# Optimization experiments

Hardware: AMD Instinct MI355X
Metric: run time of the kernel (lower is better)

The kernel has to match this reference:

```python
import jax, jax.numpy as jnp
import numpy as np

D_MODEL = 1024
N_HEADS = 16
HEAD_DIM = D_MODEL // N_HEADS
EPS = 1e-5


def _rope_tables(T, dim, dtype):
    inv_freq = 1.0 / (10000.0 ** (np.arange(0, dim, 2, dtype=np.float32) / dim))
    t = np.arange(T, dtype=np.float32)
    freqs = np.einsum('i,j->ij', t, inv_freq)            # [T, dim/2]
    emb = np.concatenate([freqs, freqs], axis=-1)        # [T, dim]
    return jnp.asarray(np.cos(emb), dtype), jnp.asarray(np.sin(emb), dtype)


def _rotate(x, cos, sin):
    # x: [B, T, H, hd]; cos/sin: [T, hd] broadcast over B, H
    c = cos[None, :, None, :]
    s = sin[None, :, None, :]
    x1, x2 = jnp.split(x, 2, axis=-1)
    return x * c + jnp.concatenate([-x2, x1], axis=-1) * s


def setup_inputs() -> dict:
    key = jax.random.key(0)
    k1, k2, k3 = jax.random.split(key, 3)
    B, T = 2, 2048
    x = jax.random.normal(k1, (B, T, D_MODEL), jnp.float32)
    norm_w = jnp.ones((D_MODEL,), jnp.float32)
    w_qkv = jax.random.normal(k2, (D_MODEL, 3 * D_MODEL), jnp.float32) * (D_MODEL ** -0.5)
    w_out = jax.random.normal(k3, (D_MODEL, D_MODEL), jnp.float32) * (D_MODEL ** -0.5)
    return {"x": x, "norm_w": norm_w, "w_qkv": w_qkv, "w_out": w_out}


def reference(x, norm_w, w_qkv, w_out):
    B, T, D = x.shape
    residual = x
    # RMSNorm
    h = x * jax.lax.rsqrt(jnp.mean(x * x, axis=-1, keepdims=True) + EPS) * norm_w
    # QKV projection
    qkv = (h @ w_qkv).reshape(B, T, 3, N_HEADS, HEAD_DIM)
    q, k, v = qkv[:, :, 0], qkv[:, :, 1], qkv[:, :, 2]   # [B, T, H, hd]
    # RoPE
    cos, sin = _rope_tables(T, HEAD_DIM, x.dtype)
    q = _rotate(q, cos, sin)
    k = _rotate(k, cos, sin)
    # Non-causal scaled dot-product attention
    scale = HEAD_DIM ** -0.5
    scores = jnp.einsum('bqhd,bkhd->bhqk', q, k) * scale
    attn = jax.nn.softmax(scores, axis=-1)
    out = jnp.einsum('bhqk,bkhd->bqhd', attn, v).reshape(B, T, D)
    return residual + out @ w_out
```

## Files before the change

kernel.cpp:

```cpp
#include <hip/hip_runtime.h>
#include <hip/hip_bf16.h>

typedef float f32x4 __attribute__((ext_vector_type(4)));
typedef __bf16 bf16x8 __attribute__((ext_vector_type(8)));
typedef __bf16 bf16x4 __attribute__((ext_vector_type(4)));

#define D_MODEL 1024
#define T_SEQ   2048
#define NH      16
#define HD      64

__device__ __forceinline__ void gload16(const void* g, void* l) {
    __builtin_amdgcn_global_load_lds(
        (const __attribute__((address_space(1))) unsigned int*)g,
        (__attribute__((address_space(3))) unsigned int*)l, 16, 0, 0);
}

__global__ __launch_bounds__(256) void k_rope_table(float2* __restrict__ tab) {
    int idx = blockIdx.x * 256 + threadIdx.x;
    int t = idx >> 5, i = idx & 31;
    float inv = __builtin_amdgcn_exp2f(-(float)i * 0.41524101186f);
    float ang = (float)t * inv;
    tab[idx] = make_float2(cosf(ang), sinf(ang));
}

__global__ __launch_bounds__(256) void k_rmsnorm(const float* __restrict__ x,
                                                 const float* __restrict__ w,
                                                 __bf16* __restrict__ h) {
    int row = blockIdx.x;
    int tid = threadIdx.x;
    const float4 v = ((const float4*)(x + (size_t)row * D_MODEL))[tid];
    float ss = v.x * v.x + v.y * v.y + v.z * v.z + v.w * v.w;
#pragma unroll
    for (int off = 32; off > 0; off >>= 1) ss += __shfl_down(ss, off, 64);
    __shared__ float red[4];
    if ((tid & 63) == 0) red[tid >> 6] = ss;
    __syncthreads();
    float total = red[0] + red[1] + red[2] + red[3];
    float rms = rsqrtf(total * (1.f / 1024.f) + 1e-5f);
    const float4 wv = ((const float4*)w)[tid];
    bf16x4 o;
    o[0] = (__bf16)(v.x * rms * wv.x);
    o[1] = (__bf16)(v.y * rms * wv.y);
    o[2] = (__bf16)(v.z * rms * wv.z);
    o[3] = (__bf16)(v.w * rms * wv.w);
    ((bf16x4*)(h + (size_t)row * D_MODEL))[tid] = o;
}

__global__ __launch_bounds__(256) void k_transpose_cast(const float* __restrict__ src,
                                                        __bf16* __restrict__ dst,
                                                        int R, int C) {
    __shared__ float tile[32][33];
    int tx = threadIdx.x & 31, ty = threadIdx.x >> 5;
    int c0 = blockIdx.x * 32, r0 = blockIdx.y * 32;
#pragma unroll
    for (int dy = 0; dy < 32; dy += 8)
        tile[ty + dy][tx] = src[(size_t)(r0 + ty + dy) * C + c0 + tx];
    __syncthreads();
#pragma unroll
    for (int dy = 0; dy < 32; dy += 8)
        dst[(size_t)(c0 + ty + dy) * R + r0 + tx] = (__bf16)tile[tx][ty + dy];
}

template <int EPI>
__global__ __launch_bounds__(256) void k_gemm(const __bf16* __restrict__ A,
                                              const __bf16* __restrict__ Bt, int K,
                                              const float2* __restrict__ tab,
                                              __bf16* __restrict__ Qr,
                                              __bf16* __restrict__ Kr,
                                              __bf16* __restrict__ Vt,
                                              const float* __restrict__ resid,
                                              float* __restrict__ outf) {
    __shared__ __bf16 ldsA[128 * 64];
    __shared__ __bf16 ldsB[128 * 64];
    const int tid  = threadIdx.x;
    const int lane = tid & 63;
    const int wave = tid >> 6;
    const int tile_m = blockIdx.y * 128;
    const int tile_n = blockIdx.x * 128;
    const int wm = (wave >> 1) * 64;
    const int wn = (wave & 1) * 64;
    f32x4 acc[4][4] = {};

    const int srow8 = lane >> 3;
    const int sslot = lane & 7;

    for (int k0 = 0; k0 < K; k0 += 64) {
#pragma unroll
        for (int i = 0; i < 4; i++) {
            int rbase = i * 32 + wave * 8;
            int row = rbase + srow8;
            int scol = (sslot ^ (row & 7)) * 8;
            gload16(A  + (size_t)(tile_m + row) * K + k0 + scol,
                    (char*)ldsA + rbase * 128);
            gload16(Bt + (size_t)(tile_n + row) * K + k0 + scol,
                    (char*)ldsB + rbase * 128);
        }
        __syncthreads();
#pragma unroll
        for (int kc = 0; kc < 2; kc++) {
            bf16x8 af[4], bfr[4];
            int s = kc * 4 + (lane >> 4);
#pragma unroll
            for (int mi = 0; mi < 4; mi++) {
                int row = wm + mi * 16 + (lane & 15);
                af[mi] = *(const bf16x8*)((char*)ldsA + row * 128 + ((s ^ (row & 7)) << 4));
            }
#pragma unroll
            for (int nf = 0; nf < 4; nf++) {
                int row = wn + nf * 16 + (lane & 15);
                bfr[nf] = *(const bf16x8*)((char*)ldsB + row * 128 + ((s ^ (row & 7)) << 4));
            }
#pragma unroll
            for (int mi = 0; mi < 4; mi++)
#pragma unroll
                for (int nf = 0; nf < 4; nf++)
                    acc[mi][nf] = __builtin_amdgcn_mfma_f32_16x16x32_bf16(
                        af[mi], bfr[nf], acc[mi][nf], 0, 0, 0);
        }
        __syncthreads();
    }

    if (EPI == 0) {
        const int nb  = tile_n + wn;
        const int sec = nb >> 10;
        const int hh  = (nb & 1023) >> 6;
        if (sec < 2) {
            __bf16* dstbase = (sec == 0) ? Qr : Kr;
            const float sc = (sec == 0) ? 0.180336880111f : 1.0f;
#pragma unroll
            for (int mi = 0; mi < 4; mi++) {
#pragma unroll
                for (int r = 0; r < 4; r++) {
                    int m = tile_m + wm + mi * 16 + (lane >> 4) * 4 + r;
                    int bb = m >> 11, t = m & 2047;
                    float2 cs0 = tab[t * 32 + (lane & 15)];
                    float2 cs1 = tab[t * 32 + 16 + (lane & 15)];
                    float x0 = acc[mi][0][r], x1 = acc[mi][1][r];
                    float x2 = acc[mi][2][r], x3 = acc[mi][3][r];
                    __bf16* dst = dstbase + ((size_t)(bb * NH + hh) * T_SEQ + t) * HD + (lane & 15);
                    dst[0]  = (__bf16)((x0 * cs0.x - x2 * cs0.y) * sc);
                    dst[16] = (__bf16)((x1 * cs1.x - x3 * cs1.y) * sc);
                    dst[32] = (__bf16)((x2 * cs0.x + x0 * cs0.y) * sc);
                    dst[48] = (__bf16)((x3 * cs1.x + x1 * cs1.y) * sc);
                }
            }
        } else {
#pragma unroll
            for (int mi = 0; mi < 4; mi++) {
                int m0 = tile_m + wm + mi * 16 + (lane >> 4) * 4;
                int bb = m0 >> 11, t0 = m0 & 2047;
#pragma unroll
                for (int nf = 0; nf < 4; nf++) {
                    int d = nf * 16 + (lane & 15);
                    bf16x4 pv;
                    pv[0] = (__bf16)acc[mi][nf][0];
                    pv[1] = (__bf16)acc[mi][nf][1];
                    pv[2] = (__bf16)acc[mi][nf][2];
                    pv[3] = (__bf16)acc[mi][nf][3];
                    *(bf16x4*)(Vt + ((size_t)(bb * NH + hh) * HD + d) * T_SEQ + t0) = pv;
                }
            }
        }
    } else {
#pragma unroll
        for (int mi = 0; mi < 4; mi++)
#pragma unroll
            for (int r = 0; r < 4; r++) {
                int m = tile_m + wm + mi * 16 + (lane >> 4) * 4 + r;
#pragma unroll
                for (int nf = 0; nf < 4; nf++) {
                    int n = tile_n + wn + nf * 16 + (lane & 15);
                    size_t idx = (size_t)m * D_MODEL + n;
                    outf[idx] = resid[idx] + acc[mi][nf][r];
                }
            }
    }
}

__global__ __launch_bounds__(256, 3) void k_attn(const __bf16* __restrict__ Qr,
                                                 const __bf16* __restrict__ Kr,
                                                 const __bf16* __restrict__ Vt,
                                                 __bf16* __restrict__ aout) {
    __shared__ __bf16 ldsK[2][64 * 64];
    __shared__ __bf16 ldsV[2][64 * 64];
    __shared__ __bf16 plds_all[4][32 * 64];
    const int lane = threadIdx.x & 63;
    const int wave = threadIdx.x >> 6;
    const int g  = lane >> 4;
    const int lr = lane & 15;

    const int lin = blockIdx.x;
    const int xcd = lin & 7;
    const int idx = lin >> 3;
    const int bh  = xcd * 4 + (idx >> 4);
    const int qb  = idx & 15;
    const int q0  = qb * 128 + wave * 32;

    const __bf16* Q  = Qr + (size_t)bh * T_SEQ * HD;
    const __bf16* Kp = Kr + (size_t)bh * T_SEQ * HD;
    const __bf16* Vp = Vt + (size_t)bh * HD * T_SEQ;
    char* plds = (char*)plds_all[wave];
    char* Kbase = (char*)&ldsK[0][0];
    char* Vbase = (char*)&ldsV[0][0];

    int kofs[2][4], pwr[4], prd[2];
#pragma unroll
    for (int kc = 0; kc < 2; kc++)
#pragma unroll
        for (int i = 0; i < 4; i++) {
            int row = i * 16 + lr;
            kofs[kc][i] = row * 128 + ((kc * 64 + g * 16) ^ ((row & 7) << 4));
        }
#pragma unroll
    for (int ki = 0; ki < 4; ki++)
        pwr[ki] = lr * 128 + ((ki * 32 + g * 8) ^ ((lr & 7) << 4));
#pragma unroll
    for (int kc = 0; kc < 2; kc++)
        prd[kc] = lr * 128 + ((kc * 64 + g * 16) ^ ((lr & 7) << 4));

    const int srow8 = lane >> 3;
    const int sslot = lane & 7;
    const int scol = (sslot ^ srow8) * 8;
    const int c0 = wave * 2, c1 = wave * 2 + 1;
    const int r0 = c0 * 8 + srow8, r1 = c1 * 8 + srow8;
    const __bf16* kg0 = Kp + (size_t)r0 * HD + scol;
    const __bf16* kg1 = Kp + (size_t)r1 * HD + scol;
    const __bf16* vg0 = Vp + (size_t)r0 * T_SEQ + scol;
    const __bf16* vg1 = Vp + (size_t)r1 * T_SEQ + scol;
    char* Kl0 = Kbase + c0 * 1024;
    char* Kl1 = Kbase + c1 * 1024;
    char* Vl0 = Vbase + c0 * 1024;
    char* Vl1 = Vbase + c1 * 1024;

    bf16x8 qf[2][2];
#pragma unroll
    for (int qi = 0; qi < 2; qi++)
#pragma unroll
        for (int kc = 0; kc < 2; kc++)
            qf[qi][kc] = *(const bf16x8*)(Q + (size_t)(q0 + qi * 16 + lr) * HD +
                                          kc * 32 + g * 8);

    f32x4 o[2][4] = {};
    float mrun[2] = {-1e30f, -1e30f};
    float lrun[2] = {0.f, 0.f};

    gload16(kg0, Kl0); gload16(kg1, Kl1);
    gload16(vg0, Vl0); gload16(vg1, Vl1);
    kg0 += 64 * HD; kg1 += 64 * HD; vg0 += 64; vg1 += 64;
    __syncthreads();

    for (int tile = 0; tile < 32; tile++) {
        const int bufoff = (tile & 1) << 13;
        if (tile < 31) {
            const int nb = bufoff ^ 8192;
            gload16(kg0, Kl0 + nb); gload16(kg1, Kl1 + nb);
            gload16(vg0, Vl0 + nb); gload16(vg1, Vl1 + nb);
            kg0 += 64 * HD; kg1 += 64 * HD; vg0 += 64; vg1 += 64;
        }

        f32x4 s[2][4];
        __builtin_amdgcn_s_setprio(1);
#pragma unroll
        for (int kc = 0; kc < 2; kc++) {
            bf16x8 kf[4];
#pragma unroll
            for (int ki = 0; ki < 4; ki++)
                kf[ki] = *(const bf16x8*)(Kbase + bufoff + kofs[kc][ki]);
#pragma unroll
            for (int qi = 0; qi < 2; qi++)
#pragma unroll
                for (int ki = 0; ki < 4; ki++)
                    s[qi][ki] = (kc == 0)
                        ? __builtin_amdgcn_mfma_f32_16x16x32_bf16(
                              kf[ki], qf[qi][0], f32x4{0.f, 0.f, 0.f, 0.f}, 0, 0, 0)
                        : __builtin_amdgcn_mfma_f32_16x16x32_bf16(
                              kf[ki], qf[qi][1], s[qi][ki], 0, 0, 0);
        }
        __builtin_amdgcn_s_setprio(0);

        float ts2[2];
#pragma unroll
        for (int qi = 0; qi < 2; qi++) {
            float t0 = fmaxf(fmaxf(s[qi][0][0], s[qi][0][1]), fmaxf(s[qi][0][2], s[qi][0][3]));
            float t1 = fmaxf(fmaxf(s[qi][1][0], s[qi][1][1]), fmaxf(s[qi][1][2], s[qi][1][3]));
            float t2 = fmaxf(fmaxf(s[qi][2][0], s[qi][2][1]), fmaxf(s[qi][2][2], s[qi][2][3]));
            float t3 = fmaxf(fmaxf(s[qi][3][0], s[qi][3][1]), fmaxf(s[qi][3][2], s[qi][3][3]));
            float tv = fmaxf(fmaxf(t0, t1), fmaxf(t2, t3));
            tv = fmaxf(tv, __shfl_xor(tv, 16, 64));
            tv = fmaxf(tv, __shfl_xor(tv, 32, 64));
            if (!__all(tv - mrun[qi] <= 8.f)) {
                float mnew = fmaxf(mrun[qi], tv);
                float fac = __builtin_amdgcn_exp2f(mrun[qi] - mnew);
                mrun[qi] = mnew;
                float facT[4];
#pragma unroll
                for (int r = 0; r < 4; r++)
                    facT[r] = __shfl(fac, g * 4 + r, 64);
#pragma unroll
                for (int nf = 0; nf < 4; nf++)
#pragma unroll
                    for (int r = 0; r < 4; r++)
                        o[qi][nf][r] *= facT[r];
                lrun[qi] *= fac;
            }
            float ts = 0.f;
#pragma unroll
            for (int ki = 0; ki < 4; ki++) {
                float p0 = __builtin_amdgcn_exp2f(s[qi][ki][0] - mrun[qi]);
                float p1 = __builtin_amdgcn_exp2f(s[qi][ki][1] - mrun[qi]);
                float p2 = __builtin_amdgcn_exp2f(s[qi][ki][2] - mrun[qi]);
                float p3 = __builtin_amdgcn_exp2f(s[qi][ki][3] - mrun[qi]);
                ts += (p0 + p1) + (p2 + p3);
                bf16x4 pk;
                pk[0] = (__bf16)p0; pk[1] = (__bf16)p1;
                pk[2] = (__bf16)p2; pk[3] = (__bf16)p3;
                *(bf16x4*)(plds + qi * 2048 + pwr[ki]) = pk;
            }
            ts2[qi] = ts;
        }
#pragma unroll
        for (int qi = 0; qi < 2; qi++) {
            float ts = ts2[qi];
            ts += __shfl_xor(ts, 16, 64);
            ts += __shfl_xor(ts, 32, 64);
            lrun[qi] += ts;
        }

        __builtin_amdgcn_s_setprio(1);
#pragma unroll
        for (int kc = 0; kc < 2; kc++) {
            bf16x8 vf[4];
#pragma unroll
            for (int nf = 0; nf < 4; nf++)
                vf[nf] = *(const bf16x8*)(Vbase + bufoff + kofs[kc][nf]);
            bf16x8 pf0 = *(const bf16x8*)(plds + prd[kc]);
            bf16x8 pf1 = *(const bf16x8*)(plds + 2048 + prd[kc]);
#pragma unroll
            for (int nf = 0; nf < 4; nf++)
                o[0][nf] = __builtin_amdgcn_mfma_f32_16x16x32_bf16(pf0, vf[nf], o[0][nf], 0, 0, 0);
#pragma unroll
            for (int nf = 0; nf < 4; nf++)
                o[1][nf] = __builtin_amdgcn_mfma_f32_16x16x32_bf16(pf1, vf[nf], o[1][nf], 0, 0, 0);
        }
        __builtin_amdgcn_s_setprio(0);
        __syncthreads();
    }

    const int bb = bh >> 4, hh = bh & 15;
#pragma unroll
    for (int qi = 0; qi < 2; qi++) {
        float invT[4];
#pragma unroll
        for (int r = 0; r < 4; r++)
            invT[r] = 1.f / __shfl(lrun[qi], g * 4 + r, 64);
#pragma unroll
        for (int r = 0; r < 4; r++) {
            int t = q0 + qi * 16 + g * 4 + r;
#pragma unroll
            for (int nf = 0; nf < 4; nf++) {
                int d = nf * 16 + lr;
                aout[((size_t)(bb * T_SEQ + t)) * D_MODEL + hh * HD + d] =
                    (__bf16)(o[qi][nf][r] * invT[r]);
            }
        }
    }
}

extern "C" void kernel_launch(void* const* d_in, const int* in_sizes, int n_in,
                              void* d_out, int out_size, void* d_ws, size_t ws_size,
                              hipStream_t stream) {
    const float* x      = (const float*)d_in[0];
    const float* norm_w = (const float*)d_in[1];
    const float* w_qkv  = (const float*)d_in[2];
    const float* w_out  = (const float*)d_in[3];
    float* out = (float*)d_out;
    char* ws = (char*)d_ws;

    __bf16* hbuf  = (__bf16*)(ws);
    __bf16* wqkvT = (__bf16*)(ws + ((size_t)8  << 20));
    __bf16* woutT = (__bf16*)(ws + ((size_t)14 << 20));
    float2* tab   = (float2*)(ws + ((size_t)16 << 20));
    __bf16* Qr    = (__bf16*)(ws + ((size_t)17 << 20));
    __bf16* Kr    = (__bf16*)(ws + ((size_t)25 << 20));
    __bf16* Vt    = (__bf16*)(ws + ((size_t)33 << 20));

    k_rope_table<<<dim3(256), dim3(256), 0, stream>>>(tab);
    k_rmsnorm<<<dim3(4096), dim3(256), 0, stream>>>(x, norm_w, hbuf);
    k_transpose_cast<<<dim3(96, 32), dim3(256), 0, stream>>>(w_qkv, wqkvT, 1024, 3072);
    k_transpose_cast<<<dim3(32, 32), dim3(256), 0, stream>>>(w_out, woutT, 1024, 1024);
    k_gemm<0><<<dim3(24, 32), dim3(256), 0, stream>>>(hbuf, wqkvT, 1024, tab,
                                                      Qr, Kr, Vt, nullptr, nullptr);
    k_attn<<<dim3(512), dim3(256), 0, stream>>>(Qr, Kr, Vt, hbuf);
    k_gemm<1><<<dim3(8, 32), dim3(256), 0, stream>>>(hbuf, woutT, 1024, nullptr,
                                                     nullptr, nullptr, nullptr, x, out);
}
```

Before: 215.5 us.

## Merge prep kernels into one launch and remap GEMM tiles per XCD

The rope-table, RMSNorm and two weight transpose-cast kernels become one k_prep launch that picks its role by block index, removing three launches and the gaps between them. The GEMM gets a linear grid whose tile remap groups column tiles by XCD (lin & 7) for better L2 locality. The output projection switches to a 64-wide N tile, doubling its block count from 256 to 512 to fill more CUs. The trade-off is smaller per-block reuse in the output GEMM and a branchy prep kernel.

Result: faster. 205.8 us (-4.5%).

```diff
diff --git a/kernel.cpp b/kernel.cpp
--- a/kernel.cpp
+++ b/kernel.cpp
@@ -16,71 +16,84 @@
         (__attribute__((address_space(3))) unsigned int*)l, 16, 0, 0);
 }
 
-__global__ __launch_bounds__(256) void k_rope_table(float2* __restrict__ tab) {
-    int idx = blockIdx.x * 256 + threadIdx.x;
-    int t = idx >> 5, i = idx & 31;
-    float inv = __builtin_amdgcn_exp2f(-(float)i * 0.41524101186f);
-    float ang = (float)t * inv;
-    tab[idx] = make_float2(cosf(ang), sinf(ang));
+__global__ __launch_bounds__(256) void k_prep(const float* __restrict__ x,
+                                              const float* __restrict__ nw,
+                                              const float* __restrict__ w_qkv,
+                                              const float* __restrict__ w_out,
+                                              __bf16* __restrict__ h,
+                                              __bf16* __restrict__ wqkvT,
+                                              __bf16* __restrict__ woutT,
+                                              float2* __restrict__ tab) {
+    __shared__ float tile[32][33];
+    __shared__ float red[4];
+    const int b = blockIdx.x;
+    const int tid = threadIdx.x;
+
+    if (b < 4096) {
+        const float* src; __bf16* dst; int R, C, bx, by;
+        if (b < 3072) { src = w_qkv; dst = wqkvT; R = 1024; C = 3072; bx = b % 96; by = b / 96; }
+        else { int b2 = b - 3072; src = w_out; dst = woutT; R = 1024; C = 1024; bx = b2 % 32; by = b2 / 32; }
+        int tx = tid & 31, ty = tid >> 5;
+        int c0 = bx * 32, r0 = by * 32;
+#pragma unroll
+        for (int dy = 0; dy < 32; dy += 8)
+            tile[ty + dy][tx] = src[(size_t)(r0 + ty + dy) * C + c0 + tx];
+        __syncthreads();
+#pragma unroll
+        for (int dy = 0; dy < 32; dy += 8)
+            dst[(size_t)(c0 + ty + dy) * R + r0 + tx] = (__bf16)tile[tx][ty + dy];
+    } else if (b < 8192) {
+        int row = b - 4096;
+        const float4 v = ((const float4*)(x + (size_t)row * D_MODEL))[tid];
+        float ss = v.x * v.x + v.y * v.y + v.z * v.z + v.w * v.w;
+#pragma unroll
+        for (int off = 32; off > 0; off >>= 1) ss += __shfl_down(ss, off, 64);
+        if ((tid & 63) == 0) red[tid >> 6] = ss;
+        __syncthreads();
+        float total = red[0] + red[1] + red[2] + red[3];
+        float rms = rsqrtf(total * (1.f / 1024.f) + 1e-5f);
+        const float4 wv = ((const float4*)nw)[tid];
+        bf16x4 o;
+        o[0] = (__bf16)(v.x * rms * wv.x);
+        o[1] = (__bf16)(v.y * rms * wv.y);
+        o[2] = (__bf16)(v.z * rms * wv.z);
+        o[3] = (__bf16)(v.w * rms * wv.w);
+        ((bf16x4*)(h + (size_t)row * D_MODEL))[tid] = o;
+    } else {
+        int idx = (b - 8192) * 256 + tid;
+        int t = idx >> 5, i = idx & 31;
+        float inv = __builtin_amdgcn_exp2f(-(float)i * 0.41524101186f);
+        float ang = (float)t * inv;
+        tab[idx] = make_float2(cosf(ang), sinf(ang));
+    }
 }
 
-__global__ __launch_bounds__(256) void k_rmsnorm(const float* __restrict__ x,
-                                                 const float* __restrict__ w,
-                                                 __bf16* __restrict__ h) {
-    int row = blockIdx.x;
-    int tid = threadIdx.x;
-    const float4 v = ((const float4*)(x + (size_t)row * D_MODEL))[tid];
-    float ss = v.x * v.x + v.y * v.y + v.z * v.z + v.w * v.w;
-#pragma unroll
-    for (int off = 32; off > 0; off >>= 1) ss += __shfl_down(ss, off, 64);
-    __shared__ float red[4];
-    if ((tid & 63) == 0) red[tid >> 6] = ss;
-    __syncthreads();
-    float total = red[0] + red[1] + red[2] + red[3];
-    float rms = rsqrtf(total * (1.f / 1024.f) + 1e-5f);
-    const float4 wv = ((const float4*)w)[tid];
-    bf16x4 o;
-    o[0] = (__bf16)(v.x * rms * wv.x);
-    o[1] = (__bf16)(v.y * rms * wv.y);
-    o[2] = (__bf16)(v.z * rms * wv.z);
-    o[3] = (__bf16)(v.w * rms * wv.w);
-    ((bf16x4*)(h + (size_t)row * D_MODEL))[tid] = o;
-}
-
-__global__ __launch_bounds__(256) void k_transpose_cast(const float* __restrict__ src,
-                                                        __bf16* __restrict__ dst,
-                                                        int R, int C) {
-    __shared__ float tile[32][33];
-    int tx = threadIdx.x & 31, ty = threadIdx.x >> 5;
-    int c0 = blockIdx.x * 32, r0 = blockIdx.y * 32;
-#pragma unroll
-    for (int dy = 0; dy < 32; dy += 8)
-        tile[ty + dy][tx] = src[(size_t)(r0 + ty + dy) * C + c0 + tx];
-    __syncthreads();
-#pragma unroll
-    for (int dy = 0; dy < 32; dy += 8)
-        dst[(size_t)(c0 + ty + dy) * R + r0 + tx] = (__bf16)tile[tx][ty + dy];
-}
-
-template <int EPI>
+template <int EPI, int BN>
 __global__ __launch_bounds__(256) void k_gemm(const __bf16* __restrict__ A,
                                               const __bf16* __restrict__ Bt, int K,
+                                              int bxc,
                                               const float2* __restrict__ tab,
                                               __bf16* __restrict__ Qr,
                                               __bf16* __restrict__ Kr,
                                               __bf16* __restrict__ Vt,
                                               const float* __restrict__ resid,
                                               float* __restrict__ outf) {
+    constexpr int NF = BN / 32;
     __shared__ __bf16 ldsA[128 * 64];
-    __shared__ __bf16 ldsB[128 * 64];
+    __shared__ __bf16 ldsB[BN * 64];
     const int tid  = threadIdx.x;
     const int lane = tid & 63;
     const int wave = tid >> 6;
-    const int tile_m = blockIdx.y * 128;
-    const int tile_n = blockIdx.x * 128;
+    const int lin = blockIdx.x;
+    const int xcd = lin & 7;
+    const int j   = lin >> 3;
+    const int bx  = xcd * bxc + j % bxc;
+    const int by  = j / bxc;
+    const int tile_m = by * 128;
+    const int tile_n = bx * BN;
     const int wm = (wave >> 1) * 64;
-    const int wn = (wave & 1) * 64;
-    f32x4 acc[4][4] = {};
+    const int wn = (wave & 1) * (BN / 2);
+    f32x4 acc[4][NF] = {};
 
     const int srow8 = lane >> 3;
     const int sslot = lane & 7;
@@ -91,15 +104,21 @@
             int rbase = i * 32 + wave * 8;
             int row = rbase + srow8;
             int scol = (sslot ^ (row & 7)) * 8;
-            gload16(A  + (size_t)(tile_m + row) * K + k0 + scol,
+            gload16(A + (size_t)(tile_m + row) * K + k0 + scol,
                     (char*)ldsA + rbase * 128);
+        }
+#pragma unroll
+        for (int i = 0; i < BN / 32; i++) {
+            int rbase = i * 32 + wave * 8;
+            int row = rbase + srow8;
+            int scol = (sslot ^ (row & 7)) * 8;
             gload16(Bt + (size_t)(tile_n + row) * K + k0 + scol,
                     (char*)ldsB + rbase * 128);
         }
         __syncthreads();
 #pragma unroll
         for (int kc = 0; kc < 2; kc++) {
-            bf16x8 af[4], bfr[4];
+            bf16x8 af[4], bfr[NF];
             int s = kc * 4 + (lane >> 4);
 #pragma unroll
             for (int mi = 0; mi < 4; mi++) {
@@ -107,21 +126,21 @@
                 af[mi] = *(const bf16x8*)((char*)ldsA + row * 128 + ((s ^ (row & 7)) << 4));
             }
 #pragma unroll
-            for (int nf = 0; nf < 4; nf++) {
+            for (int nf = 0; nf < NF; nf++) {
                 int row = wn + nf * 16 + (lane & 15);
                 bfr[nf] = *(const bf16x8*)((char*)ldsB + row * 128 + ((s ^ (row & 7)) << 4));
             }
 #pragma unroll
             for (int mi = 0; mi < 4; mi++)
 #pragma unroll
-                for (int nf = 0; nf < 4; nf++)
+                for (int nf = 0; nf < NF; nf++)
                     acc[mi][nf] = __builtin_amdgcn_mfma_f32_16x16x32_bf16(
                         af[mi], bfr[nf], acc[mi][nf], 0, 0, 0);
         }
         __syncthreads();
     }
 
-    if (EPI == 0) {
+    if constexpr (EPI == 0) {
         const int nb  = tile_n + wn;
         const int sec = nb >> 10;
         const int hh  = (nb & 1023) >> 6;
@@ -169,7 +188,7 @@
             for (int r = 0; r < 4; r++) {
                 int m = tile_m + wm + mi * 16 + (lane >> 4) * 4 + r;
 #pragma unroll
-                for (int nf = 0; nf < 4; nf++) {
+                for (int nf = 0; nf < NF; nf++) {
                     int n = tile_n + wn + nf * 16 + (lane & 15);
                     size_t idx = (size_t)m * D_MODEL + n;
                     outf[idx] = resid[idx] + acc[mi][nf][r];
@@ -385,13 +404,11 @@
     __bf16* Kr    = (__bf16*)(ws + ((size_t)25 << 20));
     __bf16* Vt    = (__bf16*)(ws + ((size_t)33 << 20));
 
-    k_rope_table<<<dim3(256), dim3(256), 0, stream>>>(tab);
-    k_rmsnorm<<<dim3(4096), dim3(256), 0, stream>>>(x, norm_w, hbuf);
-    k_transpose_cast<<<dim3(96, 32), dim3(256), 0, stream>>>(w_qkv, wqkvT, 1024, 3072);
-    k_transpose_cast<<<dim3(32, 32), dim3(256), 0, stream>>>(w_out, woutT, 1024, 1024);
-    k_gemm<0><<<dim3(24, 32), dim3(256), 0, stream>>>(hbuf, wqkvT, 1024, tab,
-                                                      Qr, Kr, Vt, nullptr, nullptr);
+    k_prep<<<dim3(8448), dim3(256), 0, stream>>>(x, norm_w, w_qkv, w_out,
+                                                 hbuf, wqkvT, woutT, tab);
+    k_gemm<0, 128><<<dim3(768), dim3(256), 0, stream>>>(hbuf, wqkvT, 1024, 3, tab,
+                                                        Qr, Kr, Vt, nullptr, nullptr);
     k_attn<<<dim3(512), dim3(256), 0, stream>>>(Qr, Kr, Vt, hbuf);
-    k_gemm<1><<<dim3(8, 32), dim3(256), 0, stream>>>(hbuf, woutT, 1024, nullptr,
-                                                     nullptr, nullptr, nullptr, x, out);
+    k_gemm<1, 64><<<dim3(512), dim3(256), 0, stream>>>(hbuf, woutT, 1024, 2, nullptr,
+                                                       nullptr, nullptr, nullptr, x, out);
 }
```
